# Performance work log

Hardware: AMD Instinct MI355X
Metric: run time of the kernel (lower is better)

## Reference

```python
import jax, jax.numpy as jnp
import numpy as np

BS, N, D, NB = 1024, 50, 3, 10
STEP = 0.01  # sigmoid(logit(0.01))


def _mlp(x, W1, b1, W2, b2, W3, b3):
    h = jax.nn.relu(x @ W1 + b1)
    h = jax.nn.relu(h @ W2 + b2)
    return h @ W3 + b3


def _poly_library(var):
    # var: (bs, n, 3) -> (bs, n, 10): [1, x, y, z, x^2, xy, xz, y^2, yz, z^2]
    ones = jnp.ones(var.shape[:-1] + (1,), var.dtype)
    quad = jnp.stack([var[..., i] * var[..., j] for i in range(D) for j in range(i, D)], axis=-1)
    return jnp.concatenate([ones, var, quad], axis=-1)


def _build_A(h):
    # Constraint matrix for one 2nd-order ODE system with variables u[t,k], col = 3t+k.
    # Rows: N equation constraints (u1[t] = rhs[t], since coeffs=[0,1,0]),
    #       1 initial-value constraint (u0[0] = iv),
    #       2*(N-1) Taylor smoothness constraints with step sizes h[t].
    n, nv = N, 3 * N
    t = jnp.arange(n)
    s = jnp.arange(n - 1)
    A_eq = jnp.zeros((n, nv)).at[t, 3 * t + 1].set(1.0)
    A_iv = jnp.zeros((1, nv)).at[0, 0].set(1.0)
    A0 = (jnp.zeros((n - 1, nv)).at[s, 3 * (s + 1)].set(1.0)
          .at[s, 3 * s].set(-1.0).at[s, 3 * s + 1].set(-h).at[s, 3 * s + 2].set(-0.5 * h * h))
    A1 = (jnp.zeros((n - 1, nv)).at[s, 3 * (s + 1) + 1].set(1.0)
          .at[s, 3 * s + 1].set(-1.0).at[s, 3 * s + 2].set(-h))
    return jnp.concatenate([A_eq, A_iv, A0, A1], axis=0)  # (3N-1, 3N)


def _ode_solve(rhs, iv, h):
    # rhs: (N,), iv: scalar, h: (N-1,).  Min-norm solution of the underdetermined
    # constrained system A u = b (KKT solve of the ODEINDLayer program).
    A = _build_A(h)
    b = jnp.concatenate([rhs, iv[None], jnp.zeros(2 * (N - 1), rhs.dtype)])
    G = A @ A.T
    u = A.T @ jnp.linalg.solve(G, b)
    eps = jnp.sqrt(jnp.sum((A @ u - b) ** 2))  # constraint residual (slack magnitude)
    u = u.reshape(N, 3)
    return u[:, 0], u[:, 1], u[:, 2], eps


def _forward(net_iv, param_in, pW1, pb1, pW2, pb2, pW3, pb3, nW1, nb1, nW2, nb2, nW3, nb3, mask):
    bs = net_iv.shape[0]
    xi = _mlp(param_in, pW1, pb1, pW2, pb2, pW3, pb3).reshape(1, NB, D) * mask  # (1, 10, 3)
    var = _mlp(net_iv.reshape(bs, -1), nW1, nb1, nW2, nb2, nW3, nb3).reshape(bs, N, D)
    basis = _poly_library(var)                      # (bs, N, 10)
    rhs = jnp.einsum('bnk,kd->bdn', basis, xi[0])   # (bs, 3, N)
    steps = jnp.full((bs, D, N - 1), STEP, net_iv.dtype)
    iv = var[:, 0]                                  # (bs, 3)
    x0, x1, x2, eps = jax.vmap(jax.vmap(_ode_solve))(rhs, iv, steps)
    return x0.transpose(0, 2, 1), steps, eps, var, xi


def setup_inputs() -> dict:
    ks = jax.random.split(jax.random.key(0), 16)

    def lin(kw, fi, fo):
        return jax.random.normal(kw, (fi, fo), jnp.float32) / np.float32(np.sqrt(fi))

    d_in = N * D  # 150
    return {
        'net_iv': jax.random.normal(ks[0], (BS, N, D), jnp.float32),
        'param_in': jax.random.normal(ks[1], (1, 64), jnp.float32),
        'pW1': lin(ks[2], 64, 1024), 'pb1': jnp.zeros((1024,), jnp.float32),
        'pW2': lin(ks[3], 1024, 1024), 'pb2': jnp.zeros((1024,), jnp.float32),
        'pW3': lin(ks[4], 1024, NB * D), 'pb3': jnp.zeros((NB * D,), jnp.float32),
        'nW1': lin(ks[5], d_in, 1024), 'nb1': jnp.zeros((1024,), jnp.float32),
        'nW2': lin(ks[6], 1024, 1024), 'nb2': jnp.zeros((1024,), jnp.float32),
        'nW3': lin(ks[7], 1024, d_in), 'nb3': jnp.zeros((d_in,), jnp.float32),
        'mask': jnp.ones((1, NB, D), jnp.float32),
    }


def reference(net_iv, param_in, pW1, pb1, pW2, pb2, pW3, pb3, nW1, nb1, nW2, nb2, nW3, nb3, mask):
    return _forward(net_iv, param_in, pW1, pb1, pW2, pb2, pW3, pb3, nW1, nb1, nW2, nb2, nW3, nb3, mask)
```

## Files before the change

kernel.cpp:

```cpp
#include <hip/hip_runtime.h>

#define OUT0_OFF  0
#define STEPS_OFF 153600
#define EPS_OFF   304128
#define VAR_OFF   307200
#define XI_OFF    460800

typedef short bf16x8 __attribute__((ext_vector_type(8)));
typedef float f32x4  __attribute__((ext_vector_type(4)));
typedef unsigned short u16x8 __attribute__((ext_vector_type(8)));
typedef unsigned short u16x4 __attribute__((ext_vector_type(4)));

__device__ __forceinline__ unsigned short f2bf(float x) {
    union { float f; unsigned u; } c; c.f = x;
    return (unsigned short)((c.u + 0x7FFFu + ((c.u >> 16) & 1u)) >> 16);
}
__device__ __forceinline__ float bf2f(unsigned short h) {
    union { float f; unsigned u; } c; c.u = ((unsigned)h) << 16;
    return c.f;
}

__device__ __forceinline__ void fma16v(const float4& av, const float4& bv,
                                       float acc[4][4]) {
    const float a_[4] = {av.x, av.y, av.z, av.w};
    const float b_[4] = {bv.x, bv.y, bv.z, bv.w};
    #pragma unroll
    for (int i = 0; i < 4; ++i)
        #pragma unroll
        for (int j = 0; j < 4; ++j)
            acc[i][j] = fmaf(a_[i], b_[j], acc[i][j]);
}

__global__ __launch_bounds__(256)
void transp_both(const float* __restrict__ w2,
                 unsigned short* __restrict__ t2h, unsigned short* __restrict__ t2l,
                 const float* __restrict__ w3,
                 unsigned short* __restrict__ t3h, unsigned short* __restrict__ t3l,
                 const float* __restrict__ px, const float* __restrict__ pW1,
                 const float* __restrict__ pb1, float* __restrict__ h1p)
{
    __shared__ float Ts[64][65];
    const int t = threadIdx.x;

    if (blockIdx.x == 19) {
        float* red = &Ts[0][0];
        const int jl = t & 63, kg = t >> 6;
        const int j = blockIdx.y * 64 + jl;
        float acc = 0.f;
        for (int k = kg * 16; k < kg * 16 + 16; ++k)
            acc = fmaf(px[k], pW1[k * 1024 + j], acc);
        red[kg * 64 + jl] = acc;
        __syncthreads();
        if (kg == 0) {
            float s = red[jl] + red[64 + jl] + red[128 + jl] + red[192 + jl];
            h1p[j] = fmaxf(s + pb1[j], 0.f);
        }
        return;
    }

    const bool w3path = blockIdx.x >= 16;
    const int n0 = (w3path ? (blockIdx.x - 16) : blockIdx.x) * 64;
    const int k0 = blockIdx.y * 64;
    const int g = t >> 6;
    const int l = t & 63;
    #pragma unroll
    for (int i = 0; i < 16; ++i) {
        const int kl = g * 16 + i;
        if (w3path) {
            const int n = n0 + l;
            Ts[kl][l] = (n < 150) ? w3[(k0 + kl) * 150 + n] : 0.f;
        } else {
            Ts[kl][l] = w2[(k0 + kl) * 1024 + n0 + l];
        }
    }
    __syncthreads();
    unsigned short* th = w3path ? t3h : t2h;
    unsigned short* tl = w3path ? t3l : t2l;
    #pragma unroll
    for (int i = 0; i < 16; ++i) {
        const int nl = g * 16 + i;
        const float x = Ts[l][nl];
        const unsigned short h = f2bf(x);
        th[(long)(n0 + nl) * 1024 + k0 + l] = h;
        tl[(long)(n0 + nl) * 1024 + k0 + l] = f2bf(x - bf2f(h));
    }
}

__global__ __launch_bounds__(128)
void gemm1_k150(const float* __restrict__ A, const float* __restrict__ B,
                const float* __restrict__ bias,
                unsigned short* __restrict__ H1h, unsigned short* __restrict__ H1l)
{
    __shared__ __align__(16) float As[150][36];
    __shared__ __align__(16) float Bs[150][64];
    const int t = threadIdx.x;

    const int col0 = blockIdx.x * 64;
    const int row0 = blockIdx.y * 32;

    for (int i = t; i < 4800; i += 128) {
        const int r = i / 150;
        const int k = i - r * 150;
        As[k][r] = A[row0 * 150 + i];
    }
    {
        const int c4 = (t & 15) * 4;
        for (int k = t >> 4; k < 150; k += 8)
            *(float4*)&Bs[k][c4] = *(const float4*)(B + k * 1024 + col0 + c4);
    }
    __syncthreads();

    const int tx4 = (t & 15) * 4;
    const int ty4 = (t >> 4) * 4;
    float acc[4][4] = {};
    float4 aA = *(const float4*)&As[0][ty4], bA = *(const float4*)&Bs[0][tx4];
    float4 aB = *(const float4*)&As[1][ty4], bB = *(const float4*)&Bs[1][tx4];
    #pragma unroll 5
    for (int k = 0; k < 150; k += 2) {
        float4 aN0 = {}, bN0 = {}, aN1 = {}, bN1 = {};
        if (k + 2 < 150) {
            aN0 = *(const float4*)&As[k + 2][ty4];
            bN0 = *(const float4*)&Bs[k + 2][tx4];
        }
        if (k + 3 < 150) {
            aN1 = *(const float4*)&As[k + 3][ty4];
            bN1 = *(const float4*)&Bs[k + 3][tx4];
        }
        fma16v(aA, bA, acc);
        fma16v(aB, bB, acc);
        aA = aN0; bA = bN0; aB = aN1; bB = bN1;
    }
    #pragma unroll
    for (int i = 0; i < 4; ++i) {
        const int r = row0 + ty4 + i;
        #pragma unroll
        for (int j = 0; j < 4; ++j) {
            const int c = col0 + tx4 + j;
            const float v = fmaxf(acc[i][j] + bias[c], 0.f);
            const unsigned short h = f2bf(v);
            H1h[r * 1024 + c] = h;
            H1l[r * 1024 + c] = f2bf(v - bf2f(h));
        }
    }
}

__global__ __launch_bounds__(256)
void mv2_part(const float* __restrict__ h1p, const float* __restrict__ pW2,
              float* __restrict__ part)
{
    const int b = blockIdx.x;
    const int j = (b & 3) * 256 + threadIdx.x;
    const int k0 = (b >> 2) * 64;
    float a0 = 0.f, a1 = 0.f, a2 = 0.f, a3 = 0.f;
    #pragma unroll
    for (int k = k0; k < k0 + 64; k += 4) {
        a0 = fmaf(h1p[k + 0], pW2[(k + 0) * 1024 + j], a0);
        a1 = fmaf(h1p[k + 1], pW2[(k + 1) * 1024 + j], a1);
        a2 = fmaf(h1p[k + 2], pW2[(k + 2) * 1024 + j], a2);
        a3 = fmaf(h1p[k + 3], pW2[(k + 3) * 1024 + j], a3);
    }
    part[(b >> 2) * 1024 + j] = (a0 + a1) + (a2 + a3);
}

__global__ __launch_bounds__(256, 1)
void gemm2_mfma(const unsigned short* __restrict__ Ah, const unsigned short* __restrict__ Al,
                const unsigned short* __restrict__ Bh, const unsigned short* __restrict__ Bl,
                float* __restrict__ P2,
                const float* __restrict__ part, const float* __restrict__ pb2,
                float* __restrict__ hvec)
{
    __shared__ __align__(16) unsigned short L[2][4][2112];
    const int t = threadIdx.x;

    if (blockIdx.z == 2) {
        const int idx = blockIdx.y * 16 + blockIdx.x;
        if (idx >= 4) return;
        const int j = idx * 256 + t;
        float s = 0.f;
        #pragma unroll
        for (int sl2 = 0; sl2 < 16; ++sl2) s += part[sl2 * 1024 + j];
        hvec[j] = fmaxf(s + pb2[j], 0.f);
        return;
    }

    const int x = blockIdx.x, y = blockIdx.y;
    const int xcd = x & 7;
    const int v   = ((x >> 3) << 4) + y;
    const int by  = (xcd >> 1) * 4 + (v & 3);
    const int bx  = (xcd & 1) * 8 + (v >> 2);
    const int m0 = by * 64;
    const int n0 = bx * 64;
    const int K = 1024, nk = 16;
    const long kbase = (long)blockIdx.z * 512;

    const int sm = t >> 6;
    const int sl = t & 63;
    const unsigned short* src = (sm == 0) ? Ah : (sm == 1) ? Al
                              : (sm == 2) ? Bh : Bl;
    const int srow0 = (sm < 2) ? m0 : n0;

    u16x8 gv[4];
    auto stage_load = [&](int kt) {
        const long kb = kbase + (long)kt * 32;
        #pragma unroll
        for (int c2 = 0; c2 < 4; ++c2) {
            const int flat = c2 * 64 + sl;
            const int row = flat >> 2, kg = flat & 3;
            gv[c2] = *(const u16x8*)(src + (long)(srow0 + row) * K + kb + kg * 8);
        }
    };
    auto stage_write = [&](int buf) {
        #pragma unroll
        for (int c2 = 0; c2 < 4; ++c2) {
            const int flat = c2 * 64 + sl;
            const int row = flat >> 2, kg = flat & 3;
            *(u16x8*)&L[buf][sm][kg * 528 + row * 8] = gv[c2];
        }
    };

    const int wv = t >> 6;
    const int r0 = (wv >> 1) * 32, c0 = (wv & 1) * 32;
    const int lane = t & 63, lr = lane & 15, kg = lane >> 4;

    f32x4 accH[2][2] = {};
    f32x4 accL[2][2] = {};
    stage_load(0);
    stage_write(0);
    __syncthreads();
    for (int kt = 0; kt < nk; ++kt) {
        const int buf = kt & 1;
        if (kt + 1 < nk) stage_load(kt + 1);
        const short* lb = (const short*)&L[buf][0][0];
        bf16x8 fah[2], fal[2], fbh[2], fbl[2];
        #pragma unroll
        for (int rt = 0; rt < 2; ++rt) {
            const int o = kg * 528 + (r0 + rt * 16 + lr) * 8;
            fah[rt] = *(const bf16x8*)(lb + o);
            fal[rt] = *(const bf16x8*)(lb + 2112 + o);
        }
        #pragma unroll
        for (int ct = 0; ct < 2; ++ct) {
            const int o = kg * 528 + (c0 + ct * 16 + lr) * 8;
            fbh[ct] = *(const bf16x8*)(lb + 4224 + o);
            fbl[ct] = *(const bf16x8*)(lb + 6336 + o);
        }
        #pragma unroll
        for (int rt = 0; rt < 2; ++rt)
            #pragma unroll
            for (int ct = 0; ct < 2; ++ct) {
                accH[rt][ct] = __builtin_amdgcn_mfma_f32_16x16x32_bf16(
                                   fah[rt], fbh[ct], accH[rt][ct], 0, 0, 0);
                accL[rt][ct] = __builtin_amdgcn_mfma_f32_16x16x32_bf16(
                                   fah[rt], fbl[ct], accL[rt][ct], 0, 0, 0);
                accL[rt][ct] = __builtin_amdgcn_mfma_f32_16x16x32_bf16(
                                   fal[rt], fbh[ct], accL[rt][ct], 0, 0, 0);
            }
        if (kt + 1 < nk) stage_write(buf ^ 1);
        __syncthreads();
    }

    float* Cb = P2 + (long)blockIdx.z * 1048576;
    #pragma unroll
    for (int rt = 0; rt < 2; ++rt)
        #pragma unroll
        for (int ct = 0; ct < 2; ++ct)
            #pragma unroll
            for (int j = 0; j < 4; ++j)
                Cb[(long)(m0 + r0 + rt * 16 + kg * 4 + j) * 1024 +
                   (n0 + c0 + ct * 16 + lr)] = accH[rt][ct][j] + accL[rt][ct][j];
}

__global__ __launch_bounds__(256, 1)
void gemm3_mfma(const float* __restrict__ P2, const float* __restrict__ nb2,
                const unsigned short* __restrict__ Bh, const unsigned short* __restrict__ Bl,
                float* __restrict__ P3,
                const float* __restrict__ hvec,
                const float* __restrict__ pW3, const float* __restrict__ pb3,
                const float* __restrict__ mask, float* __restrict__ xi)
{
    __shared__ __align__(16) unsigned short L[2][4][2112];
    const int t = threadIdx.x;

    const int g   = blockIdx.x;
    const int sk  = blockIdx.y;
    const int bxi = (g >> 3) & 3;
    const int by  = (g & 7) + ((g >> 5) << 3);

    if (bxi == 3) {
        const int idx = by * 8 + sk;
        if (idx >= 15) return;
        const int j = idx * 2 + (t >> 7);
        const int lane = t & 127;
        float acc = 0.f;
        for (int k = lane; k < 1024; k += 128)
            acc = fmaf(hvec[k], pW3[k * 30 + j], acc);
        #pragma unroll
        for (int off = 32; off > 0; off >>= 1) acc += __shfl_down(acc, off, 64);
        float* red = (float*)&L[0][0][0];
        if ((t & 63) == 0) red[t >> 6] = acc;
        __syncthreads();
        if ((t & 127) == 0)
            xi[j] = (red[t >> 6] + red[(t >> 6) + 1] + pb3[j]) * mask[j];
        return;
    }

    const int m0 = by * 64;
    const int n0 = bxi * 64;
    const int nk = 4;
    const long kbase = (long)sk * 128;

    float4 ga[2][2];
    u16x8 gb[2];
    auto stage_load = [&](int kt) {
        const long kb = kbase + (long)kt * 32;
        #pragma unroll
        for (int c = 0; c < 2; ++c) {
            const int idx = c * 256 + t;
            const int row = idx >> 3, q = idx & 7;
            const long o = (long)(m0 + row) * 1024 + kb + q * 4;
            float4 p = *(const float4*)(P2 + o);
            float4 s = *(const float4*)(P2 + 1048576 + o);
            float4 bv = *(const float4*)(nb2 + kb + q * 4);
            ga[c][0].x = p.x + s.x + bv.x; ga[c][0].y = p.y + s.y + bv.y;
            ga[c][0].z = p.z + s.z + bv.z; ga[c][0].w = p.w + s.w + bv.w;
            ga[c][1] = ga[c][0];
        }
        {
            const int row = t >> 2, kg = t & 3;
            const long o = (long)(n0 + row) * 1024 + kb + kg * 8;
            gb[0] = *(const u16x8*)(Bh + o);
            gb[1] = *(const u16x8*)(Bl + o);
        }
    };
    auto stage_write = [&](int buf) {
        #pragma unroll
        for (int c = 0; c < 2; ++c) {
            const int idx = c * 256 + t;
            const int row = idx >> 3, q = idx & 7;
            const float v[4] = {fmaxf(ga[c][0].x, 0.f), fmaxf(ga[c][0].y, 0.f),
                                fmaxf(ga[c][0].z, 0.f), fmaxf(ga[c][0].w, 0.f)};
            u16x4 hh, ll;
            hh.x = f2bf(v[0]); ll.x = f2bf(v[0] - bf2f(hh.x));
            hh.y = f2bf(v[1]); ll.y = f2bf(v[1] - bf2f(hh.y));
            hh.z = f2bf(v[2]); ll.z = f2bf(v[2] - bf2f(hh.z));
            hh.w = f2bf(v[3]); ll.w = f2bf(v[3] - bf2f(hh.w));
            const int kg = q >> 1, half = (q & 1) * 4;
            *(u16x4*)&L[buf][0][kg * 528 + row * 8 + half] = hh;
            *(u16x4*)&L[buf][1][kg * 528 + row * 8 + half] = ll;
        }
        {
            const int row = t >> 2, kg = t & 3;
            *(u16x8*)&L[buf][2][kg * 528 + row * 8] = gb[0];
            *(u16x8*)&L[buf][3][kg * 528 + row * 8] = gb[1];
        }
    };

    const int wv = t >> 6;
    const int r0 = (wv >> 1) * 32, c0 = (wv & 1) * 32;
    const int lane = t & 63, lr = lane & 15, kg = lane >> 4;

    f32x4 accH[2][2] = {};
    f32x4 accL[2][2] = {};
    stage_load(0);
    stage_write(0);
    __syncthreads();
    for (int kt = 0; kt < nk; ++kt) {
        const int buf = kt & 1;
        if (kt + 1 < nk) stage_load(kt + 1);
        const short* lb = (const short*)&L[buf][0][0];
        bf16x8 fah[2], fal[2], fbh[2], fbl[2];
        #pragma unroll
        for (int rt = 0; rt < 2; ++rt) {
            const int o = kg * 528 + (r0 + rt * 16 + lr) * 8;
            fah[rt] = *(const bf16x8*)(lb + o);
            fal[rt] = *(const bf16x8*)(lb + 2112 + o);
        }
        #pragma unroll
        for (int ct = 0; ct < 2; ++ct) {
            const int o = kg * 528 + (c0 + ct * 16 + lr) * 8;
            fbh[ct] = *(const bf16x8*)(lb + 4224 + o);
            fbl[ct] = *(const bf16x8*)(lb + 6336 + o);
        }
        #pragma unroll
        for (int rt = 0; rt < 2; ++rt)
            #pragma unroll
            for (int ct = 0; ct < 2; ++ct) {
                accH[rt][ct] = __builtin_amdgcn_mfma_f32_16x16x32_bf16(
                                   fah[rt], fbh[ct], accH[rt][ct], 0, 0, 0);
                accL[rt][ct] = __builtin_amdgcn_mfma_f32_16x16x32_bf16(
                                   fah[rt], fbl[ct], accL[rt][ct], 0, 0, 0);
                accL[rt][ct] = __builtin_amdgcn_mfma_f32_16x16x32_bf16(
                                   fal[rt], fbh[ct], accL[rt][ct], 0, 0, 0);
            }
        if (kt + 1 < nk) stage_write(buf ^ 1);
        __syncthreads();
    }

    float* Cb = P3 + (long)sk * 196608;
    #pragma unroll
    for (int rt = 0; rt < 2; ++rt)
        #pragma unroll
        for (int ct = 0; ct < 2; ++ct)
            #pragma unroll
            for (int j = 0; j < 4; ++j)
                Cb[(long)(m0 + r0 + rt * 16 + kg * 4 + j) * 192 +
                   (n0 + c0 + ct * 16 + lr)] = accH[rt][ct][j] + accL[rt][ct][j];
}

__global__ __launch_bounds__(256)
void ode_kernel(const float* __restrict__ P3, const float* __restrict__ nb3,
                const float* __restrict__ xi, float* __restrict__ varp,
                float* __restrict__ out0, float* __restrict__ steps,
                float* __restrict__ eps)
{
    const int t  = threadIdx.x;
    const int bl = t >> 6;
    const int b  = blockIdx.x * 4 + bl;
    const int lt = t & 63;
    __shared__ float s_var[4][152];
    __shared__ float s_xi[30];
    __shared__ float s_rhs[4][50][3];
    if (t < 30) s_xi[t] = xi[t];
    for (int i = lt; i < 150; i += 64) {
        float v = nb3[i];
        #pragma unroll
        for (int s = 0; s < 8; ++s) v += P3[s * 196608 + b * 192 + i];
        s_var[bl][i] = v;
        varp[b * 150 + i] = v;
    }
    __syncthreads();
    if (lt < 50) {
        const float v0 = s_var[bl][lt * 3 + 0];
        const float v1 = s_var[bl][lt * 3 + 1];
        const float v2 = s_var[bl][lt * 3 + 2];
        const float bas[10] = {1.f, v0, v1, v2,
                               v0 * v0, v0 * v1, v0 * v2,
                               v1 * v1, v1 * v2, v2 * v2};
        #pragma unroll
        for (int d = 0; d < 3; ++d) {
            float r = 0.f;
            #pragma unroll
            for (int k = 0; k < 10; ++k) r = fmaf(bas[k], s_xi[k * 3 + d], r);
            s_rhs[bl][lt][d] = r;
        }
    }
    __syncthreads();
    if (lt < 3) {
        float x = s_var[bl][lt];
        out0[b * 150 + lt] = x;
        for (int n = 1; n < 50; ++n) {
            x = fmaf(0.005f, s_rhs[bl][n - 1][lt] + s_rhs[bl][n][lt], x);
            out0[b * 150 + n * 3 + lt] = x;
        }
        eps[b * 3 + lt] = 0.f;
    }
    for (int i = lt; i < 147; i += 64) steps[b * 147 + i] = 0.01f;
}

extern "C" void kernel_launch(void* const* d_in, const int* in_sizes, int n_in,
                              void* d_out, int out_size, void* d_ws, size_t ws_size,
                              hipStream_t stream)
{
    const float* net_iv   = (const float*)d_in[0];
    const float* param_in = (const float*)d_in[1];
    const float* pW1 = (const float*)d_in[2];
    const float* pb1 = (const float*)d_in[3];
    const float* pW2 = (const float*)d_in[4];
    const float* pb2 = (const float*)d_in[5];
    const float* pW3 = (const float*)d_in[6];
    const float* pb3 = (const float*)d_in[7];
    const float* nW1 = (const float*)d_in[8];
    const float* nb1 = (const float*)d_in[9];
    const float* nW2 = (const float*)d_in[10];
    const float* nb2 = (const float*)d_in[11];
    const float* nW3 = (const float*)d_in[12];
    const float* nb3 = (const float*)d_in[13];
    const float* mask= (const float*)d_in[14];

    float* out = (float*)d_out;
    float* out0p  = out + OUT0_OFF;
    float* stepsp = out + STEPS_OFF;
    float* epsp   = out + EPS_OFF;
    float* varp   = out + VAR_OFF;
    float* xip    = out + XI_OFF;

    unsigned short* H1h  = (unsigned short*)d_ws;
    unsigned short* H1l  = H1h + 1048576;
    unsigned short* W2Th = H1l + 1048576;
    unsigned short* W2Tl = W2Th + 1048576;
    unsigned short* B3Th = W2Tl + 1048576;
    unsigned short* B3Tl = B3Th + 196608;
    float* P2   = (float*)(B3Tl + 196608);
    float* P3   = P2 + 2097152;
    float* part = P3 + 1572864;
    float* hvec = part + 16384;
    float* h1p  = hvec + 1024;

    hipLaunchKernelGGL(transp_both, dim3(20, 16), dim3(256), 0, stream,
                       nW2, W2Th, W2Tl, nW3, B3Th, B3Tl,
                       param_in, pW1, pb1, h1p);

    hipLaunchKernelGGL(gemm1_k150, dim3(16, 32), dim3(128), 0, stream,
                       net_iv, nW1, nb1, H1h, H1l);

    hipLaunchKernelGGL(mv2_part, dim3(64), dim3(256), 0, stream,
                       h1p, pW2, part);

    hipLaunchKernelGGL(gemm2_mfma, dim3(16, 16, 3), dim3(256), 0, stream,
                       H1h, H1l, W2Th, W2Tl, P2, part, pb2, hvec);

    hipLaunchKernelGGL(gemm3_mfma, dim3(64, 8), dim3(256), 0, stream,
                       P2, nb2, B3Th, B3Tl, P3, hvec, pW3, pb3, mask, xip);

    hipLaunchKernelGGL(ode_kernel, dim3(256), dim3(256), 0, stream,
                       P3, nb3, xip, varp, out0p, stepsp, epsp);
}
```

Measured before the change: 57.52 us.

## Split split-K reduce+bias+relu+bf16 split into separate kernel before gemm3

Moves the reduction of the two split-K partials of gemm2, the bias add, ReLU and hi/lo bf16 splitting out of gemm3's staging loop into a dedicated elementwise kernel writing H2h/H2l. Gemm3 then loads plain bf16 tiles with one uniform vector-load path per wave, removing redundant per-tile recomputation, since each A tile was previously re-reduced by all three column blocks. This costs an extra kernel launch and an extra write and read of the 4 MB bf16 activations.

```diff
diff --git a/kernel.cpp b/kernel.cpp
--- a/kernel.cpp
+++ b/kernel.cpp
@@ -270,8 +270,30 @@
                    (n0 + c0 + ct * 16 + lr)] = accH[rt][ct][j] + accL[rt][ct][j];
 }
 
+__global__ __launch_bounds__(256)
+void reduce2s(const float* __restrict__ P, const float* __restrict__ bias,
+              unsigned short* __restrict__ H2h, unsigned short* __restrict__ H2l)
+{
+    const int i4 = blockIdx.x * 256 + threadIdx.x;
+    float4 p = ((const float4*)P)[i4];
+    float4 q = ((const float4*)(P + 1048576))[i4];
+    const int c0 = (i4 << 2) & 1023;
+    float4 bv = *(const float4*)&bias[c0];
+    float v0 = fmaxf(p.x + q.x + bv.x, 0.f);
+    float v1 = fmaxf(p.y + q.y + bv.y, 0.f);
+    float v2 = fmaxf(p.z + q.z + bv.z, 0.f);
+    float v3 = fmaxf(p.w + q.w + bv.w, 0.f);
+    u16x4 hh, ll;
+    hh.x = f2bf(v0); ll.x = f2bf(v0 - bf2f(hh.x));
+    hh.y = f2bf(v1); ll.y = f2bf(v1 - bf2f(hh.y));
+    hh.z = f2bf(v2); ll.z = f2bf(v2 - bf2f(hh.z));
+    hh.w = f2bf(v3); ll.w = f2bf(v3 - bf2f(hh.w));
+    *(u16x4*)&H2h[(long)i4 << 2] = hh;
+    *(u16x4*)&H2l[(long)i4 << 2] = ll;
+}
+
 __global__ __launch_bounds__(256, 1)
-void gemm3_mfma(const float* __restrict__ P2, const float* __restrict__ nb2,
+void gemm3_mfma(const unsigned short* __restrict__ Ah, const unsigned short* __restrict__ Al,
                 const unsigned short* __restrict__ Bh, const unsigned short* __restrict__ Bl,
                 float* __restrict__ P3,
                 const float* __restrict__ hvec,
@@ -306,52 +328,31 @@
 
     const int m0 = by * 64;
     const int n0 = bxi * 64;
-    const int nk = 4;
+    const int K = 1024, nk = 4;
     const long kbase = (long)sk * 128;
 
-    float4 ga[2][2];
-    u16x8 gb[2];
+    const int sm = t >> 6;
+    const int sl = t & 63;
+    const unsigned short* src = (sm == 0) ? Ah : (sm == 1) ? Al
+                              : (sm == 2) ? Bh : Bl;
+    const int srow0 = (sm < 2) ? m0 : n0;
+
+    u16x8 gv[4];
     auto stage_load = [&](int kt) {
         const long kb = kbase + (long)kt * 32;
         #pragma unroll
-        for (int c = 0; c < 2; ++c) {
-            const int idx = c * 256 + t;
-            const int row = idx >> 3, q = idx & 7;
-            const long o = (long)(m0 + row) * 1024 + kb + q * 4;
-            float4 p = *(const float4*)(P2 + o);
-            float4 s = *(const float4*)(P2 + 1048576 + o);
-            float4 bv = *(const float4*)(nb2 + kb + q * 4);
-            ga[c][0].x = p.x + s.x + bv.x; ga[c][0].y = p.y + s.y + bv.y;
-            ga[c][0].z = p.z + s.z + bv.z; ga[c][0].w = p.w + s.w + bv.w;
-            ga[c][1] = ga[c][0];
-        }
-        {
-            const int row = t >> 2, kg = t & 3;
-            const long o = (long)(n0 + row) * 1024 + kb + kg * 8;
-            gb[0] = *(const u16x8*)(Bh + o);
-            gb[1] = *(const u16x8*)(Bl + o);
+        for (int c2 = 0; c2 < 4; ++c2) {
+            const int flat = c2 * 64 + sl;
+            const int row = flat >> 2, kg = flat & 3;
+            gv[c2] = *(const u16x8*)(src + (long)(srow0 + row) * K + kb + kg * 8);
         }
     };
     auto stage_write = [&](int buf) {
         #pragma unroll
-        for (int c = 0; c < 2; ++c) {
-            const int idx = c * 256 + t;
-            const int row = idx >> 3, q = idx & 7;
-            const float v[4] = {fmaxf(ga[c][0].x, 0.f), fmaxf(ga[c][0].y, 0.f),
-                                fmaxf(ga[c][0].z, 0.f), fmaxf(ga[c][0].w, 0.f)};
-            u16x4 hh, ll;
-            hh.x = f2bf(v[0]); ll.x = f2bf(v[0] - bf2f(hh.x));
-            hh.y = f2bf(v[1]); ll.y = f2bf(v[1] - bf2f(hh.y));
-            hh.z = f2bf(v[2]); ll.z = f2bf(v[2] - bf2f(hh.z));
-            hh.w = f2bf(v[3]); ll.w = f2bf(v[3] - bf2f(hh.w));
-            const int kg = q >> 1, half = (q & 1) * 4;
-            *(u16x4*)&L[buf][0][kg * 528 + row * 8 + half] = hh;
-            *(u16x4*)&L[buf][1][kg * 528 + row * 8 + half] = ll;
-        }
-        {
-            const int row = t >> 2, kg = t & 3;
-            *(u16x8*)&L[buf][2][kg * 528 + row * 8] = gb[0];
-            *(u16x8*)&L[buf][3][kg * 528 + row * 8] = gb[1];
+        for (int c2 = 0; c2 < 4; ++c2) {
+            const int flat = c2 * 64 + sl;
+            const int row = flat >> 2, kg = flat & 3;
+            *(u16x8*)&L[buf][sm][kg * 528 + row * 8] = gv[c2];
         }
     };
 
@@ -488,7 +489,9 @@
     unsigned short* H1l  = H1h + 1048576;
     unsigned short* W2Th = H1l + 1048576;
     unsigned short* W2Tl = W2Th + 1048576;
-    unsigned short* B3Th = W2Tl + 1048576;
+    unsigned short* H2h  = W2Tl + 1048576;
+    unsigned short* H2l  = H2h + 1048576;
+    unsigned short* B3Th = H2l + 1048576;
     unsigned short* B3Tl = B3Th + 196608;
     float* P2   = (float*)(B3Tl + 196608);
     float* P3   = P2 + 2097152;
@@ -509,8 +512,11 @@
     hipLaunchKernelGGL(gemm2_mfma, dim3(16, 16, 3), dim3(256), 0, stream,
                        H1h, H1l, W2Th, W2Tl, P2, part, pb2, hvec);
 
+    hipLaunchKernelGGL(reduce2s, dim3(1024), dim3(256), 0, stream,
+                       P2, nb2, H2h, H2l);
+
     hipLaunchKernelGGL(gemm3_mfma, dim3(64, 8), dim3(256), 0, stream,
-                       P2, nb2, B3Th, B3Tl, P3, hvec, pW3, pb3, mask, xip);
+                       H2h, H2l, B3Th, B3Tl, P3, hvec, pW3, pb3, mask, xip);
 
     hipLaunchKernelGGL(ode_kernel, dim3(256), dim3(256), 0, stream,
                        P3, nb3, xip, varp, out0p, stepsp, epsp);
```

After: 60.02 us. 1.04x slower.
